# Optimization experiments

Hardware: AMD Instinct MI355X
Metric: run time of the kernel (lower is better)

The kernel has to match this reference:

```python
import jax, jax.numpy as jnp
import numpy as np

N = 65536
D_IN = 784
H = 20
D_OUT = 10
N_MID = 28  # fc2..fc29, all Linear(20,20)


def setup_inputs() -> dict:
    key = jax.random.key(0)
    ks = jax.random.split(key, 8)
    # PyTorch Linear default init: U(-1/sqrt(fan_in), 1/sqrt(fan_in)); uniform is fine for a reference.
    def uni(k, shape, fan_in):
        bound = 1.0 / np.sqrt(fan_in)
        return jax.random.uniform(k, shape, jnp.float32, -bound, bound)
    x = jax.random.normal(ks[0], (N, D_IN), jnp.float32)
    W1 = uni(ks[1], (H, D_IN), D_IN)
    b1 = uni(ks[2], (H,), D_IN)
    Wmid = uni(ks[3], (N_MID, H, H), H)   # stacked fc2..fc29 weights
    bmid = uni(ks[4], (N_MID, H), H)
    W30 = uni(ks[5], (D_OUT, H), H)
    b30 = uni(ks[6], (D_OUT,), H)
    return {"x": x, "W1": W1, "b1": b1, "Wmid": Wmid, "bmid": bmid, "W30": W30, "b30": b30}


def reference(x, W1, b1, Wmid, bmid, W30, b30):
    # fc1 + relu
    h = jax.nn.relu(x @ W1.T + b1)  # [N, 20]
    # fc2..fc29 + relu, identical structure -> scan over stacked params
    def step(h, wb):
        W, b = wb
        return jax.nn.relu(h @ W.T + b), None
    h, _ = jax.lax.scan(step, h, (Wmid, bmid))
    # fc30 (no relu)
    return h @ W30.T + b30  # [N, 10]
```

## Files before the change

### kernel.cpp

```cpp
#include <hip/hip_runtime.h>

typedef __attribute__((ext_vector_type(8))) short short8;
typedef __attribute__((ext_vector_type(16))) float f32x16;
typedef unsigned short ushort_t;

#define MFMA(A, B, C) __builtin_amdgcn_mfma_f32_32x32x16_bf16(A, B, C, 0, 0, 0)

__device__ __forceinline__ float4 ldf4(const float* p) { return *(const float4*)p; }
__device__ __forceinline__ short8 ld8(const void* p) { return *(const short8*)p; }

__device__ __forceinline__ short8 mk8(unsigned w0, unsigned w1, unsigned w2, unsigned w3) {
    union { unsigned u[4]; short8 s; } t;
    t.u[0] = w0; t.u[1] = w1; t.u[2] = w2; t.u[3] = w3;
    return t.s;
}
__device__ __forceinline__ unsigned packhi2(float a, float b) {
    return __builtin_amdgcn_perm(__float_as_uint(b), __float_as_uint(a), 0x07060302u);
}
__device__ __forceinline__ float lopart(float v) {
    return v - __uint_as_float(__float_as_uint(v) & 0xFFFF0000u);
}
__device__ __forceinline__ void plswap(unsigned& lo, unsigned& hi) {
    asm("v_permlane32_swap_b32 %0, %1" : "+v"(lo), "+v"(hi));
}
__device__ __forceinline__ ushort_t h16(float x) { return (ushort_t)(__float_as_uint(x) >> 16); }
__device__ __forceinline__ float fh(ushort_t u) { return __uint_as_float(((unsigned)u) << 16); }

__device__ __forceinline__ void dma16(const float* g, void* l) {
    __builtin_amdgcn_global_load_lds((const __attribute__((address_space(1))) void*)g,
                                     (__attribute__((address_space(3))) void*)l, 16, 0, 0);
}

__global__ void prepack(const float* __restrict__ W1,
                        const float* __restrict__ Wmid, const float* __restrict__ bmid,
                        const float* __restrict__ W30, const float* __restrict__ b30,
                        ushort_t* __restrict__ w1t, ushort_t* __restrict__ midt)
{
    const int tid = blockIdx.x * 256 + threadIdx.x;
    const int nth = gridDim.x * 256;
    for (int i = tid; i < 49 * 512; i += nth) {
        const int j = i & 7, hf = (i >> 3) & 1, o = (i >> 4) & 31, s = i >> 9;
        const float v = (o < 20) ? W1[o * 784 + s * 16 + hf * 8 + j] : 0.f;
        w1t[i] = h16(v);
    }
    for (int e2 = tid; e2 < 29 * 64; e2 += nth) {
        const int ee = e2 & 63, l = e2 >> 6;
        const int o = ee & 31, hf = ee >> 5;
        ushort_t v[32];
#pragma unroll
        for (int i = 0; i < 32; ++i) v[i] = 0;
        const bool lastl = (l == 28);
        const int omax = lastl ? 10 : 20;
        if (o < omax) {
            const float* wr = lastl ? (W30 + o * 20) : (Wmid + l * 400 + o * 20);
            const float bias = lastl ? b30[o] : bmid[l * 20 + o];
#pragma unroll
            for (int j = 0; j < 8; ++j) {
                const float w = wr[hf * 8 + j];
                v[j]      = h16(w);
                v[16 + j] = h16(w - fh(h16(w)));
            }
            if (hf == 0) {
#pragma unroll
                for (int j = 0; j < 4; ++j) {
                    const float w = wr[16 + j];
                    v[8 + j]  = h16(w);
                    v[24 + j] = h16(w - fh(h16(w)));
                }
                v[12] = h16(bias);
                v[13] = h16(bias - fh(h16(bias)));
            }
        }
#pragma unroll
        for (int f = 0; f < 4; ++f)
#pragma unroll
            for (int j = 0; j < 8; ++j)
                midt[l * 2048 + f * 512 + ee * 8 + j] = v[f * 8 + j];
    }
}

__global__ __launch_bounds__(256, 4)
void mlp_main(const float* __restrict__ x, const float* __restrict__ b1,
              const ushort_t* __restrict__ w1t, const ushort_t* __restrict__ midt,
              float* __restrict__ out, int nrows)
{
    __shared__ float xt[2][4096];
    __shared__ float xtail[2048];

    const int tid  = threadIdx.x;
    const int lane = tid & 63;
    const int wv   = tid >> 6;
    const int r0   = blockIdx.x * 128;
    if (r0 >= nrows) return;
    const int colr = lane & 31;
    const int half = lane >> 5;
    const int rsw  = colr & 7;
    const int row  = r0 + wv * 32 + colr;
    const int rw0  = r0 + wv * 32;

#define ISSUE_PHASE(PH, BUF) do {                                          \
        char* _lb = (char*)&xt[(BUF)][wv * 1024];                          \
        const int _pc = (PH) * 32;                                         \
        _Pragma("unroll")                                                  \
        for (int k = 0; k < 4; ++k) {                                      \
            const int slot = k * 64 + lane;                    \
            const int rl = slot >> 3, gs = slot & 7;                       \
            const int g = gs ^ (rl & 7);                                   \
            const size_t gr = (size_t)((rw0 + rl < nrows) ? (rw0 + rl) : (nrows - 1)); \
            dma16(x + gr * 784 + _pc + g * 4, _lb + k * 1024);             \
        }                                                                  \
    } while (0)

#pragma unroll
    for (int k = 0; k < 2; ++k) {
        const int slot = k * 64 + lane;
        const int rl = slot >> 2, u = slot & 3;
        const size_t gr = (size_t)((rw0 + rl < nrows) ? (rw0 + rl) : (nrows - 1));
        dma16(x + gr * 784 + 768 + u * 4, (char*)xtail + wv * 2048 + k * 1024);
    }
    ISSUE_PHASE(0, 0);

    f32x16 acc;
#pragma unroll
    for (int r = 0; r < 16; ++r) acc[r] = 0.f;

#pragma unroll 1
    for (int p = 0; p < 24; ++p) {
        const ushort_t* ab = w1t + (p * 2) * 512 + colr * 16 + half * 8;
        const short8 A0 = ld8(ab);
        const short8 A1 = ld8(ab + 512);

        if (p < 23) {
            ISSUE_PHASE(p + 1, (p + 1) & 1);
            asm volatile("s_waitcnt vmcnt(4)" ::: "memory");
        } else {
            asm volatile("s_waitcnt vmcnt(0)" ::: "memory");
        }
        __builtin_amdgcn_sched_barrier(0);

        const float* xl = &xt[p & 1][wv * 1024 + colr * 32];
#pragma unroll
        for (int s = 0; s < 2; ++s) {
            const int g = s * 4 + half * 2;
            const float4 va = *(const float4*)&xl[((g)     ^ rsw) * 4];
            const float4 vb = *(const float4*)&xl[((g + 1) ^ rsw) * 4];
            const short8 B = mk8(packhi2(va.x, va.y), packhi2(va.z, va.w),
                                 packhi2(vb.x, vb.y), packhi2(vb.z, vb.w));
            acc = MFMA(s == 0 ? A0 : A1, B, acc);
        }
    }

    {
        const short8 At = ld8(w1t + 48 * 512 + colr * 16 + half * 8);
        const float* tl = &xtail[wv * 512 + colr * 16];
        const float4 va = ldf4(&tl[(half * 2) * 4]);
        const float4 vb = ldf4(&tl[(half * 2 + 1) * 4]);
        const short8 B = mk8(packhi2(va.x, va.y), packhi2(va.z, va.w),
                             packhi2(vb.x, vb.y), packhi2(vb.z, vb.w));
        acc = MFMA(At, B, acc);
    }

    float Hv[16];
#pragma unroll
    for (int r = 0; r < 16; ++r) {
        const int o = (r & 3) + 8 * (r >> 2) + 4 * half;
        Hv[r] = fmaxf(acc[r] + b1[o < 20 ? o : 0], 0.f);
    }

    const ushort_t* ap = midt + lane * 8;
#pragma unroll 1
    for (int l = 0; l < 29; ++l) {
        const short8 A0h = ld8(ap + l * 2048);
        const short8 A1h = ld8(ap + l * 2048 + 512);
        const short8 A0l = ld8(ap + l * 2048 + 1024);
        const short8 A1l = ld8(ap + l * 2048 + 1536);

        unsigned plo0 = packhi2(Hv[0], Hv[1]), plo1 = packhi2(Hv[2], Hv[3]);
        unsigned phi0 = packhi2(Hv[4], Hv[5]), phi1 = packhi2(Hv[6], Hv[7]);
        plswap(plo0, phi0); plswap(plo1, phi1);
        const short8 B0h = mk8(plo0, plo1, phi0, phi1);

        unsigned qlo0 = packhi2(lopart(Hv[0]), lopart(Hv[1]));
        unsigned qlo1 = packhi2(lopart(Hv[2]), lopart(Hv[3]));
        unsigned qhi0 = packhi2(lopart(Hv[4]), lopart(Hv[5]));
        unsigned qhi1 = packhi2(lopart(Hv[6]), lopart(Hv[7]));
        plswap(qlo0, qhi0); plswap(qlo1, qhi1);
        const short8 B0l = mk8(qlo0, qlo1, qhi0, qhi1);

        const short8 B1h = mk8(half ? 0u : packhi2(Hv[8], Hv[9]),
                               half ? 0u : packhi2(Hv[10], Hv[11]),
                               half ? 0u : 0x00003F80u, 0u);
        const short8 B1l = mk8(half ? 0u : packhi2(lopart(Hv[8]), lopart(Hv[9])),
                               half ? 0u : packhi2(lopart(Hv[10]), lopart(Hv[11])),
                               half ? 0u : 0x3F800000u, 0u);

        f32x16 d;
#pragma unroll
        for (int r = 0; r < 16; ++r) d[r] = 0.f;
        d = MFMA(A0h, B0h, d);
        d = MFMA(A0l, B0h, d);
        d = MFMA(A0h, B0l, d);
        d = MFMA(A1h, B1h, d);
        d = MFMA(A1l, B1h, d);
        d = MFMA(A1h, B1l, d);

        if (l < 28) {
#pragma unroll
            for (int r = 0; r < 16; ++r) Hv[r] = fmaxf(d[r], 0.f);
        } else {
            if (row < nrows) {
#pragma unroll
                for (int r = 0; r < 16; ++r) {
                    const int o = (r & 3) + 8 * (r >> 2) + 4 * half;
                    if (o < 10) out[(size_t)row * 10 + o] = d[r];
                }
            }
        }
    }
#undef ISSUE_PHASE
}

extern "C" void kernel_launch(void* const* d_in, const int* in_sizes, int n_in,
                              void* d_out, int out_size, void* d_ws, size_t ws_size,
                              hipStream_t stream)
{
    const float* x    = (const float*)d_in[0];
    const float* W1   = (const float*)d_in[1];
    const float* b1   = (const float*)d_in[2];
    const float* Wmid = (const float*)d_in[3];
    const float* bmid = (const float*)d_in[4];
    const float* W30  = (const float*)d_in[5];
    const float* b30  = (const float*)d_in[6];
    float* out = (float*)d_out;

    ushort_t* w1t  = (ushort_t*)d_ws;
    ushort_t* midt = (ushort_t*)((char*)d_ws + 50176);

    const int nrows = in_sizes[0] / 784;
    prepack<<<32, 256, 0, stream>>>(W1, Wmid, bmid, W30, b30, w1t, midt);
    const int grid = (nrows + 127) / 128;
    mlp_main<<<grid, 256, 0, stream>>>(x, b1, w1t, midt, out, nrows);
}
```

Measured before the change: 52.07 us.

## Deepen fc1 x-load pipeline to four LDS stages with prefetched weight fragments

Replaces the double-buffered fc1 loop with a four-slot ring. Async DMA of x tiles and the bf16 W1 fragment loads are issued three phases ahead, with explicit vmcnt waits. The loop is unrolled by four so slot indices are compile-time constants. This aims to hide global memory latency better per wave, but doubles LDS use and lowers the launch-bounds occupancy hint from 4 to 2 blocks per CU, which reduces latency hiding from other waves.

New measurement: 52.20 us. Within noise of the previous version (+0.2%).

```diff
diff --git a/kernel.cpp b/kernel.cpp
--- a/kernel.cpp
+++ b/kernel.cpp
@@ -79,12 +79,12 @@
     }
 }
 
-__global__ __launch_bounds__(256, 4)
+__global__ __launch_bounds__(256, 2)
 void mlp_main(const float* __restrict__ x, const float* __restrict__ b1,
               const ushort_t* __restrict__ w1t, const ushort_t* __restrict__ midt,
               float* __restrict__ out, int nrows)
 {
-    __shared__ float xt[2][4096];
+    __shared__ float xt[4][4096];
     __shared__ float xtail[2048];
 
     const int tid  = threadIdx.x;
@@ -111,6 +111,36 @@
         }                                                                  \
     } while (0)
 
+#define ALOAD(IP, ISLOT) do {                                              \
+        const ushort_t* _ab = w1t + ((IP) * 2) * 512 + colr * 16 + half * 8; \
+        A0r[(ISLOT)] = ld8(_ab);                                           \
+        A1r[(ISLOT)] = ld8(_ab + 512);                                     \
+    } while (0)
+
+#define PHASE(P, SLOT, IP, ISLOT, VMSTR) do {                              \
+        if ((IP) >= 0) { ISSUE_PHASE((IP), (ISLOT)); ALOAD((IP), (ISLOT)); } \
+        __builtin_amdgcn_sched_barrier(0);                                 \
+        asm volatile("s_waitcnt vmcnt(" VMSTR ")" ::: "memory");           \
+        __builtin_amdgcn_sched_barrier(0);                                 \
+        {                                                                  \
+            const float* _xl = &xt[(SLOT)][wv * 1024 + colr * 32];         \
+            _Pragma("unroll")                                              \
+            for (int s = 0; s < 2; ++s) {                                  \
+                const int g = s * 4 + half * 2;                            \
+                const float4 va = *(const float4*)&_xl[((g)     ^ rsw) * 4]; \
+                const float4 vb = *(const float4*)&_xl[((g + 1) ^ rsw) * 4]; \
+                const short8 B = mk8(packhi2(va.x, va.y), packhi2(va.z, va.w), \
+                                     packhi2(vb.x, vb.y), packhi2(vb.z, vb.w)); \
+                acc = MFMA(s == 0 ? A0r[(SLOT)] : A1r[(SLOT)], B, acc);    \
+            }                                                              \
+        }                                                                  \
+    } while (0)
+
+    short8 A0r[4], A1r[4];
+    f32x16 acc;
+#pragma unroll
+    for (int r = 0; r < 16; ++r) acc[r] = 0.f;
+
 #pragma unroll
     for (int k = 0; k < 2; ++k) {
         const int slot = k * 64 + lane;
@@ -118,37 +148,25 @@
         const size_t gr = (size_t)((rw0 + rl < nrows) ? (rw0 + rl) : (nrows - 1));
         dma16(x + gr * 784 + 768 + u * 4, (char*)xtail + wv * 2048 + k * 1024);
     }
-    ISSUE_PHASE(0, 0);
-
-    f32x16 acc;
-#pragma unroll
-    for (int r = 0; r < 16; ++r) acc[r] = 0.f;
+    __builtin_amdgcn_sched_barrier(0);
+    ISSUE_PHASE(0, 0); ALOAD(0, 0);
+    __builtin_amdgcn_sched_barrier(0);
+    ISSUE_PHASE(1, 1); ALOAD(1, 1);
+    __builtin_amdgcn_sched_barrier(0);
+    ISSUE_PHASE(2, 2); ALOAD(2, 2);
 
 #pragma unroll 1
-    for (int p = 0; p < 24; ++p) {
-        const ushort_t* ab = w1t + (p * 2) * 512 + colr * 16 + half * 8;
-        const short8 A0 = ld8(ab);
-        const short8 A1 = ld8(ab + 512);
-
-        if (p < 23) {
-            ISSUE_PHASE(p + 1, (p + 1) & 1);
-            asm volatile("s_waitcnt vmcnt(4)" ::: "memory");
-        } else {
-            asm volatile("s_waitcnt vmcnt(0)" ::: "memory");
-        }
-        __builtin_amdgcn_sched_barrier(0);
-
-        const float* xl = &xt[p & 1][wv * 1024 + colr * 32];
-#pragma unroll
-        for (int s = 0; s < 2; ++s) {
-            const int g = s * 4 + half * 2;
-            const float4 va = *(const float4*)&xl[((g)     ^ rsw) * 4];
-            const float4 vb = *(const float4*)&xl[((g + 1) ^ rsw) * 4];
-            const short8 B = mk8(packhi2(va.x, va.y), packhi2(va.z, va.w),
-                                 packhi2(vb.x, vb.y), packhi2(vb.z, vb.w));
-            acc = MFMA(s == 0 ? A0 : A1, B, acc);
-        }
-    }
+    for (int pb = 0; pb < 5; ++pb) {
+        const int p0 = pb * 4;
+        PHASE(p0 + 0, 0, p0 + 3, 3, "18");
+        PHASE(p0 + 1, 1, p0 + 4, 0, "18");
+        PHASE(p0 + 2, 2, p0 + 5, 1, "18");
+        PHASE(p0 + 3, 3, p0 + 6, 2, "18");
+    }
+    PHASE(20, 0, 23, 3, "18");
+    PHASE(21, 1, -1, 0, "12");
+    PHASE(22, 2, -1, 0, "6");
+    PHASE(23, 3, -1, 0, "0");
 
     {
         const short8 At = ld8(w1t + 48 * 512 + colr * 16 + half * 8);
@@ -217,6 +235,8 @@
             }
         }
     }
+#undef PHASE
+#undef ALOAD
 #undef ISSUE_PHASE
 }
 
```
